# Performance work log

Measured on AMD Instinct MI355X. Metric: run time of the kernel, lower is better.

The kernel has to match this reference:

```python
import jax, jax.numpy as jnp
import numpy as np

B, S, H = 2, 1024, 2048
NH, NKV, HD = 16, 8, 128
GROUPS = NH // NKV
THETA = 1000000.0
SPARSITY = 0.4  # q_len > 512 -> vision_sparse_attention_sparsity_ratio
TOP_K = max(1, min(S, int(SPARSITY * S)))


def _rope(q, k, position_ids):
    # inv_freq: [HD/2]
    inv_freq = 1.0 / (THETA ** (jnp.arange(0, HD, 2, dtype=jnp.float32) / HD))
    freqs = position_ids.astype(jnp.float32)[:, :, None] * inv_freq  # [B,S,HD/2]
    emb = jnp.concatenate([freqs, freqs], axis=-1)                   # [B,S,HD]
    cos = jnp.cos(emb)[:, None].astype(q.dtype)  # [B,1,S,HD] (unsqueeze_dim=1)
    sin = jnp.sin(emb)[:, None].astype(q.dtype)
    rot = lambda x: jnp.concatenate([-x[..., HD // 2:], x[..., :HD // 2]], axis=-1)
    return q * cos + rot(q) * sin, k * cos + rot(k) * sin


def setup_inputs() -> dict:
    key = jax.random.key(0)
    ks = jax.random.split(key, 10)
    sc = 0.02
    inp = {
        'hidden_states': jax.random.normal(ks[0], (B, S, H), jnp.float32),
        'wq': jax.random.normal(ks[1], (NH * HD, H), jnp.float32) * sc,
        'bq': jax.random.normal(ks[2], (NH * HD,), jnp.float32) * sc,
        'wk': jax.random.normal(ks[3], (NKV * HD, H), jnp.float32) * sc,
        'bk': jax.random.normal(ks[4], (NKV * HD,), jnp.float32) * sc,
        'wv': jax.random.normal(ks[5], (NKV * HD, H), jnp.float32) * sc,
        'bv': jax.random.normal(ks[6], (NKV * HD,), jnp.float32) * sc,
        'wo': jax.random.normal(ks[7], (H, NH * HD), jnp.float32) * sc,
        'bo': jax.random.normal(ks[8], (H,), jnp.float32) * sc,
        'position_ids': jnp.tile(jnp.arange(S, dtype=jnp.int32)[None, :], (B, 1)),
    }
    return inp


def reference(hidden_states, wq, bq, wk, bk, wv, bv, wo, bo, position_ids):
    # QKV projections -> [B, heads, S, HD]
    q = (hidden_states @ wq.T + bq).reshape(B, S, NH, HD).transpose(0, 2, 1, 3)
    k = (hidden_states @ wk.T + bk).reshape(B, S, NKV, HD).transpose(0, 2, 1, 3)
    v = (hidden_states @ wv.T + bv).reshape(B, S, NKV, HD).transpose(0, 2, 1, 3)

    q, k = _rope(q, k, position_ids)

    # GQA: repeat_interleave KV heads along head axis
    k = jnp.repeat(k, GROUPS, axis=1)
    v = jnp.repeat(v, GROUPS, axis=1)

    scores = jnp.einsum('bhqd,bhkd->bhqk', q, k) / jnp.sqrt(jnp.float32(HD))

    # VectorizedSparseAttention: keep top-k weights per query, -inf elsewhere
    topk_vals = jax.lax.top_k(scores, TOP_K)[0]          # sorted descending
    thresh = topk_vals[..., -1:]                         # k-th largest per row
    sparse = jnp.where(scores >= thresh, scores, -jnp.inf)

    probs = jax.nn.softmax(sparse.astype(jnp.float32), axis=-1).astype(q.dtype)
    attn = jnp.einsum('bhqk,bhkd->bhqd', probs, v)       # [B,NH,S,HD]
    attn = attn.transpose(0, 2, 1, 3).reshape(B, S, NH * HD)
    return attn @ wo.T + bo
```

## Files before the change

kernel.cpp:

```cpp
#include <hip/hip_runtime.h>
#include <hip/hip_bf16.h>

constexpr int B_ = 2, S_ = 1024, H_ = 2048;
constexpr int NH_ = 16, NKV_ = 8, HD_ = 128, GROUPS_ = 2;
constexpr int TOPK_ = 409;
constexpr int QSTRIDE = NH_ * HD_;
constexpr int KSTRIDE = NKV_ * HD_;
constexpr int QB_ = 16;

typedef __attribute__((ext_vector_type(8))) short short8;
typedef __attribute__((ext_vector_type(4))) float f32x4;
typedef __attribute__((ext_vector_type(4))) unsigned u32x4;
typedef __attribute__((ext_vector_type(4))) unsigned short ush4;

__device__ inline unsigned fkey(float x) {
  unsigned u = __float_as_uint(x);
  return (u & 0x80000000u) ? ~u : (u | 0x80000000u);
}
__device__ inline unsigned short bf16_rne(float x) {
  unsigned u = __float_as_uint(x);
  unsigned r = u + 0x7FFFu + ((u >> 16) & 1u);
  return (unsigned short)(r >> 16);
}
__device__ inline float bf16_to_f(unsigned short h) {
  return __uint_as_float((unsigned)h << 16);
}
__device__ inline unsigned packsplit(float x) {
  unsigned u = __float_as_uint(x);
  unsigned r = (u + 0x7FFFu + ((u >> 16) & 1u)) & 0xFFFF0000u;
  float rem = x - __uint_as_float(r);
  unsigned v = __float_as_uint(rem);
  unsigned l = (v + 0x7FFFu + ((v >> 16) & 1u)) >> 16;
  return r | l;
}

#define PERM_HI 0x07060302u
#define PERM_LO 0x05040100u

__device__ inline void unpack8(const unsigned* p, short8& hi, short8& lo) {
  u32x4 w0 = *(const u32x4*)p;
  u32x4 w1 = *(const u32x4*)(p + 4);
  u32x4 h, l;
  h.x = __builtin_amdgcn_perm(w0.y, w0.x, PERM_HI);
  h.y = __builtin_amdgcn_perm(w0.w, w0.z, PERM_HI);
  h.z = __builtin_amdgcn_perm(w1.y, w1.x, PERM_HI);
  h.w = __builtin_amdgcn_perm(w1.w, w1.z, PERM_HI);
  l.x = __builtin_amdgcn_perm(w0.y, w0.x, PERM_LO);
  l.y = __builtin_amdgcn_perm(w0.w, w0.z, PERM_LO);
  l.z = __builtin_amdgcn_perm(w1.y, w1.x, PERM_LO);
  l.w = __builtin_amdgcn_perm(w1.w, w1.z, PERM_LO);
  hi = *(short8*)&h;
  lo = *(short8*)&l;
}

__device__ inline void wave_lds_fence() {
  asm volatile("s_waitcnt lgkmcnt(0)" ::: "memory");
}

template <int TI>
__device__ __forceinline__ void gemm_split_body(
    const float* __restrict__ A, const float* __restrict__ W,
    const float* __restrict__ bias, float* __restrict__ C, int ldc, int c0,
    int K, int m0) {
  __shared__ unsigned short Ah[2][TI * 32 * 32];
  __shared__ unsigned short Al[2][TI * 32 * 32];
  __shared__ unsigned short Wh[2][128 * 32];
  __shared__ unsigned short Wl[2][128 * 32];
  const int tid = threadIdx.x;
  const int lane = tid & 63, wid = tid >> 6;
  const int wrow = (wid >> 1) * (TI * 16), wcol = (wid & 1) * 64;
  const int fm = lane & 15, quad = lane >> 4;
  const int srow = tid >> 3;
  const int skq = (tid & 7) * 4;
  f32x4 acc[TI][4] = {};
  float4 avr[TI], wvr[4];

  auto loadAW = [&](int k0) {
#pragma unroll
    for (int r = 0; r < TI; ++r)
      avr[r] = *(const float4*)&A[(size_t)(m0 + srow + 32 * r) * K + k0 + skq];
#pragma unroll
    for (int r = 0; r < 4; ++r)
      wvr[r] = *(const float4*)&W[(size_t)(srow + 32 * r) * K + k0 + skq];
  };
  auto convWrite = [&](int buf) {
#pragma unroll
    for (int r = 0; r < TI; ++r) {
      const int row = srow + 32 * r;
      const int off =
          row * 32 + ((((skq >> 3) ^ ((row >> 1) & 3)) << 3) | (skq & 7));
      unsigned short h0 = bf16_rne(avr[r].x), h1 = bf16_rne(avr[r].y),
                     h2 = bf16_rne(avr[r].z), h3 = bf16_rne(avr[r].w);
      ush4 hv; hv.x = h0; hv.y = h1; hv.z = h2; hv.w = h3;
      ush4 lv;
      lv.x = bf16_rne(avr[r].x - bf16_to_f(h0));
      lv.y = bf16_rne(avr[r].y - bf16_to_f(h1));
      lv.z = bf16_rne(avr[r].z - bf16_to_f(h2));
      lv.w = bf16_rne(avr[r].w - bf16_to_f(h3));
      *(ush4*)&Ah[buf][off] = hv;
      *(ush4*)&Al[buf][off] = lv;
    }
#pragma unroll
    for (int r = 0; r < 4; ++r) {
      const int row = srow + 32 * r;
      const int off =
          row * 32 + ((((skq >> 3) ^ ((row >> 1) & 3)) << 3) | (skq & 7));
      unsigned short g0 = bf16_rne(wvr[r].x), g1 = bf16_rne(wvr[r].y),
                     g2 = bf16_rne(wvr[r].z), g3 = bf16_rne(wvr[r].w);
      ush4 hv; hv.x = g0; hv.y = g1; hv.z = g2; hv.w = g3;
      ush4 lv;
      lv.x = bf16_rne(wvr[r].x - bf16_to_f(g0));
      lv.y = bf16_rne(wvr[r].y - bf16_to_f(g1));
      lv.z = bf16_rne(wvr[r].z - bf16_to_f(g2));
      lv.w = bf16_rne(wvr[r].w - bf16_to_f(g3));
      *(ush4*)&Wh[buf][off] = hv;
      *(ush4*)&Wl[buf][off] = lv;
    }
  };

  loadAW(0);
  convWrite(0);
  __syncthreads();
  int cur = 0;
  for (int k0 = 0; k0 < K; k0 += 32) {
    const bool more = (k0 + 32) < K;
    if (more) loadAW(k0 + 32);
    short8 ah[TI], al[TI], bh[4], bl[4];
#pragma unroll
    for (int ti = 0; ti < TI; ++ti) {
      const int r = wrow + 16 * ti + fm;
      const int off = r * 32 + ((quad ^ ((r >> 1) & 3)) << 3);
      ah[ti] = *(const short8*)&Ah[cur][off];
      al[ti] = *(const short8*)&Al[cur][off];
    }
#pragma unroll
    for (int tj = 0; tj < 4; ++tj) {
      const int r = wcol + 16 * tj + fm;
      const int off = r * 32 + ((quad ^ ((r >> 1) & 3)) << 3);
      bh[tj] = *(const short8*)&Wh[cur][off];
      bl[tj] = *(const short8*)&Wl[cur][off];
    }
#pragma unroll
    for (int ti = 0; ti < TI; ++ti)
#pragma unroll
      for (int tj = 0; tj < 4; ++tj) {
        acc[ti][tj] = __builtin_amdgcn_mfma_f32_16x16x32_bf16(
            ah[ti], bh[tj], acc[ti][tj], 0, 0, 0);
        acc[ti][tj] = __builtin_amdgcn_mfma_f32_16x16x32_bf16(
            ah[ti], bl[tj], acc[ti][tj], 0, 0, 0);
        acc[ti][tj] = __builtin_amdgcn_mfma_f32_16x16x32_bf16(
            al[ti], bh[tj], acc[ti][tj], 0, 0, 0);
      }
    if (more) convWrite(cur ^ 1);
    __syncthreads();
    cur ^= 1;
  }
#pragma unroll
  for (int tj = 0; tj < 4; ++tj) {
    float bsv = bias[wcol + 16 * tj + fm];
#pragma unroll
    for (int ti = 0; ti < TI; ++ti) {
      int mrow = m0 + wrow + 16 * ti + quad * 4;
      int ncol = c0 + wcol + 16 * tj + fm;
#pragma unroll
      for (int reg = 0; reg < 4; ++reg)
        C[(size_t)(mrow + reg) * ldc + ncol] = acc[ti][tj][reg] + bsv;
    }
  }
}

__global__ __launch_bounds__(256) void gemm_qkv(
    const float* __restrict__ hidden, const float* __restrict__ wq,
    const float* __restrict__ bq, const float* __restrict__ wk,
    const float* __restrict__ bk, const float* __restrict__ wv,
    const float* __restrict__ bv, float* __restrict__ q, float* __restrict__ k,
    float* __restrict__ v) {
  const int n0 = blockIdx.x * 128, m0 = blockIdx.y * 128;
  const float* W;
  const float* bias;
  float* C;
  int ldc, c0;
  if (n0 < QSTRIDE) {
    W = wq + (size_t)n0 * H_; bias = bq + n0; C = q; ldc = QSTRIDE; c0 = n0;
  } else if (n0 < QSTRIDE + KSTRIDE) {
    int nn = n0 - QSTRIDE;
    W = wk + (size_t)nn * H_; bias = bk + nn; C = k; ldc = KSTRIDE; c0 = nn;
  } else {
    int nn = n0 - QSTRIDE - KSTRIDE;
    W = wv + (size_t)nn * H_; bias = bv + nn; C = v; ldc = KSTRIDE; c0 = nn;
  }
  gemm_split_body<4>(hidden, W, bias, C, ldc, c0, H_, m0);
}

template <int TI>
__global__ __launch_bounds__(256) void gemm_split_k(
    const float* __restrict__ A, const float* __restrict__ W,
    const float* __restrict__ bias, float* __restrict__ C, int N, int K) {
  const int n0 = blockIdx.x * 128, m0 = blockIdx.y * (TI * 32);
  gemm_split_body<TI>(A, W + (size_t)n0 * K, bias + n0, C, N, n0, K, m0);
}

__global__ __launch_bounds__(256) void rope_pack(float* __restrict__ qtmp,
                                                 float* __restrict__ ktmp,
                                                 float* __restrict__ vtmp,
                                                 const int* __restrict__ pos_ids) {
  const int s = blockIdx.x, b = blockIdx.y;
  const int t = threadIdx.x;
  __shared__ float fsh[64];
  if (t < 64) fsh[t] = (float)(1.0 / pow(1.0e6, (double)t / 64.0));
  __syncthreads();
  const int pos = pos_ids[b * S_ + s];
#pragma unroll
  for (int it = 0; it < 8; ++it) {
    const int p = t + 256 * it;
    const int slot = p >> 6;
    const int d = p & 63;
    float* base;
    if (slot < NH_)
      base = qtmp + (size_t)(b * S_ + s) * QSTRIDE + slot * HD_;
    else if (slot < NH_ + NKV_)
      base = ktmp + (size_t)(b * S_ + s) * KSTRIDE + (slot - NH_) * HD_;
    else
      base = vtmp + (size_t)(b * S_ + s) * KSTRIDE + (slot - NH_ - NKV_) * HD_;
    float x = base[d], y = base[d + 64];
    unsigned* up = (unsigned*)base;
    if (slot < NH_ + NKV_) {
      float ang = (float)pos * fsh[d];
      float c = cosf(ang), sn = sinf(ang);
      up[d] = packsplit(x * c - y * sn);
      up[d + 64] = packsplit(y * c + x * sn);
    } else {
      up[d] = packsplit(x);
      up[d + 64] = packsplit(y);
    }
  }
}

constexpr int SCW = 1028;
constexpr int KVP = 132;

__global__ __launch_bounds__(512, 1) void attn_kernel(
    unsigned* __restrict__ qpk, const unsigned* __restrict__ kpk,
    const unsigned* __restrict__ vpk) {
  const int q0 = blockIdx.x * QB_;
  const int h = blockIdx.y, b = blockIdx.z, g = h / GROUPS_;
  const int t = threadIdx.x, lane = t & 63, wid = t >> 6;
  const int fm = lane & 15, quad = lane >> 4;

  __shared__ float sc[QB_ * SCW];
  __shared__ unsigned kvt[128 * KVP];
  __shared__ unsigned qst[QB_][KVP];
  __shared__ unsigned hist[8][256];
  __shared__ float redmx[8][QB_];
  __shared__ float Zsh[QB_];
  __shared__ unsigned prefix_sh[QB_];
  __shared__ unsigned selbin_sh[8];
  __shared__ int selkk_sh[8];
  const float scale = 0.08838834764831845f;

  const int kt = t >> 5;
  const int st = (t & 31) * 4;
  const int stsw = st ^ (((kt >> 3) & 1) << 4);

  {
    int qi = t >> 5, c4 = (t & 31) * 4;
    u32x4 v = *(const u32x4*)&qpk[(size_t)(b * S_ + q0 + qi) * QSTRIDE +
                                  h * HD_ + c4];
    *(u32x4*)&qst[qi][c4] = v;
  }
  const unsigned* kg = kpk + (size_t)(b * S_) * KSTRIDE + g * HD_;
  u32x4 pf[8];
#pragma unroll
  for (int j = 0; j < 8; ++j)
    pf[j] = *(const u32x4*)&kg[(size_t)(kt + 16 * j) * KSTRIDE + st];
  __syncthreads();

  short8 qh[4], ql[4];
#pragma unroll
  for (int ks = 0; ks < 4; ++ks)
    unpack8(&qst[fm][ks * 32 + quad * 8], qh[ks], ql[ks]);

  const int kswz = ((fm >> 3) & 1) << 4;
  f32x4 mxacc = {-1e30f, -1e30f, -1e30f, -1e30f};
  for (int tile = 0; tile < 8; ++tile) {
    if (tile) __syncthreads();
#pragma unroll
    for (int j = 0; j < 8; ++j)
      *(u32x4*)&kvt[(kt + 16 * j) * KVP + stsw] = pf[j];
    __syncthreads();
    if (tile < 7) {
#pragma unroll
      for (int j = 0; j < 8; ++j)
        pf[j] = *(const u32x4*)&kg[(size_t)((tile + 1) * 128 + kt + 16 * j) *
                                       KSTRIDE + st];
    }
    f32x4 acc = {0.f, 0.f, 0.f, 0.f};
    const int krow = wid * 16 + fm;
#pragma unroll
    for (int ks = 0; ks < 4; ++ks) {
      short8 bh, bl;
      unpack8(&kvt[krow * KVP + ((ks * 32 + quad * 8) ^ kswz)], bh, bl);
      acc = __builtin_amdgcn_mfma_f32_16x16x32_bf16(qh[ks], bh, acc, 0, 0, 0);
      acc = __builtin_amdgcn_mfma_f32_16x16x32_bf16(qh[ks], bl, acc, 0, 0, 0);
      acc = __builtin_amdgcn_mfma_f32_16x16x32_bf16(ql[ks], bh, acc, 0, 0, 0);
    }
    const int key = tile * 128 + krow;
#pragma unroll
    for (int reg = 0; reg < 4; ++reg) {
      float sval = acc[reg] * scale;
      sc[(quad * 4 + reg) * SCW + key] = sval;
      mxacc[reg] = fmaxf(mxacc[reg], sval);
    }
  }
#pragma unroll
  for (int o = 1; o < 16; o <<= 1) {
    mxacc[0] = fmaxf(mxacc[0], __shfl_xor(mxacc[0], o));
    mxacc[1] = fmaxf(mxacc[1], __shfl_xor(mxacc[1], o));
    mxacc[2] = fmaxf(mxacc[2], __shfl_xor(mxacc[2], o));
    mxacc[3] = fmaxf(mxacc[3], __shfl_xor(mxacc[3], o));
  }
  if (fm == 0) {
#pragma unroll
    for (int reg = 0; reg < 4; ++reg) redmx[wid][quad * 4 + reg] = mxacc[reg];
  }
  __syncthreads();

  const unsigned* vg = vpk + (size_t)(b * S_) * KSTRIDE + g * HD_;
  u32x4 vf[8];
#pragma unroll
  for (int j = 0; j < 8; ++j)
    vf[j] = *(const u32x4*)&vg[(size_t)(kt + 16 * j) * KSTRIDE + st];

  for (int sq = 0; sq < 2; ++sq) {
    const int qi = wid * 2 + sq;
    int kk = TOPK_;
    unsigned prefix = 0;
    for (int pass = 0; pass < 4; ++pass) {
      const int shift = 24 - 8 * pass;
      const unsigned pmask = pass ? (0xFFFFFFFFu << (shift + 8)) : 0u;
      *(u32x4*)&hist[wid][4 * lane] = (u32x4){0, 0, 0, 0};
      wave_lds_fence();
#pragma unroll 4
      for (int j = 0; j < 16; ++j) {
        unsigned u = fkey(sc[qi * SCW + lane + 64 * j]);
        if ((u & pmask) == (prefix & pmask))
          atomicAdd(&hist[wid][(u >> shift) & 255], 1u);
      }
      wave_lds_fence();
      u32x4 cw = *(const u32x4*)&hist[wid][4 * lane];
      int c0 = (int)cw.x, c1 = (int)cw.y, c2 = (int)cw.z, c3 = (int)cw.w;
      int s3 = c3, s2 = c2 + s3, s1 = c1 + s2, s0 = c0 + s1;
      int tot = s0;
      int suf = tot;
#pragma unroll
      for (int off = 1; off < 64; off <<= 1) {
        int vv = __shfl_down(suf, off);
        if (lane + off < 64) suf += vv;
      }
      int above_lanes = suf - tot;
      int i0 = s0 + above_lanes, i1 = s1 + above_lanes;
      int i2 = s2 + above_lanes, i3 = s3 + above_lanes;
      if (i3 >= kk && i3 - c3 < kk) {
        selbin_sh[wid] = (unsigned)(4 * lane + 3); selkk_sh[wid] = kk - (i3 - c3);
      }
      if (i2 >= kk && i2 - c2 < kk) {
        selbin_sh[wid] = (unsigned)(4 * lane + 2); selkk_sh[wid] = kk - (i2 - c2);
      }
      if (i1 >= kk && i1 - c1 < kk) {
        selbin_sh[wid] = (unsigned)(4 * lane + 1); selkk_sh[wid] = kk - (i1 - c1);
      }
      if (i0 >= kk && i0 - c0 < kk) {
        selbin_sh[wid] = (unsigned)(4 * lane + 0); selkk_sh[wid] = kk - (i0 - c0);
      }
      wave_lds_fence();
      prefix |= selbin_sh[wid] << shift;
      kk = selkk_sh[wid];
    }
    if (lane == 0) prefix_sh[qi] = prefix;
  }
  wave_lds_fence();

  {
    const int qi = t >> 5, li = t & 31;
    const float mx =
        fmaxf(fmaxf(fmaxf(redmx[0][qi], redmx[1][qi]),
                    fmaxf(redmx[2][qi], redmx[3][qi])),
              fmaxf(fmaxf(redmx[4][qi], redmx[5][qi]),
                    fmaxf(redmx[6][qi], redmx[7][qi])));
    const unsigned pref = prefix_sh[qi];
    unsigned* scp = (unsigned*)&sc[qi * SCW];
    float zloc = 0.f;
#pragma unroll 2
    for (int j = 0; j < 8; ++j) {
      int i4 = li * 4 + 128 * j;
      f32x4 sv = *(const f32x4*)&sc[qi * SCW + i4];
      u32x4 pk;
      float p0 = (fkey(sv.x) >= pref) ? __expf(sv.x - mx) : 0.0f;
      float p1 = (fkey(sv.y) >= pref) ? __expf(sv.y - mx) : 0.0f;
      float p2 = (fkey(sv.z) >= pref) ? __expf(sv.z - mx) : 0.0f;
      float p3 = (fkey(sv.w) >= pref) ? __expf(sv.w - mx) : 0.0f;
      zloc += p0 + p1 + p2 + p3;
      pk.x = packsplit(p0); pk.y = packsplit(p1);
      pk.z = packsplit(p2); pk.w = packsplit(p3);
      *(u32x4*)&scp[i4] = pk;
    }
#pragma unroll
    for (int off = 1; off < 32; off <<= 1) zloc += __shfl_xor(zloc, off);
    if (li == 0) Zsh[qi] = zloc;
  }

  const unsigned* scp2 = (const unsigned*)sc;
  f32x4 oacc = {0.f, 0.f, 0.f, 0.f};
  const int dim = wid * 16 + fm;
  for (int tile = 0; tile < 8; ++tile) {
    __syncthreads();
#pragma unroll
    for (int j = 0; j < 8; ++j)
      *(u32x4*)&kvt[(kt + 16 * j) * KVP + stsw] = vf[j];
    __syncthreads();
    if (tile < 7) {
#pragma unroll
      for (int j = 0; j < 8; ++j)
        vf[j] = *(const u32x4*)&vg[(size_t)((tile + 1) * 128 + kt + 16 * j) *
                                       KSTRIDE + st];
    }
    const int dsw = dim ^ ((quad & 1) << 4);
#pragma unroll
    for (int ks = 0; ks < 4; ++ks) {
      short8 ph, pl;
      unpack8(&scp2[fm * SCW + tile * 128 + ks * 32 + quad * 8], ph, pl);
      const int rb = ks * 32 + quad * 8;
      unsigned w0 = kvt[(rb + 0) * KVP + dsw];
      unsigned w1 = kvt[(rb + 1) * KVP + dsw];
      unsigned w2 = kvt[(rb + 2) * KVP + dsw];
      unsigned w3 = kvt[(rb + 3) * KVP + dsw];
      unsigned w4 = kvt[(rb + 4) * KVP + dsw];
      unsigned w5 = kvt[(rb + 5) * KVP + dsw];
      unsigned w6 = kvt[(rb + 6) * KVP + dsw];
      unsigned w7 = kvt[(rb + 7) * KVP + dsw];
      u32x4 hq, lq;
      hq.x = __builtin_amdgcn_perm(w1, w0, PERM_HI);
      hq.y = __builtin_amdgcn_perm(w3, w2, PERM_HI);
      hq.z = __builtin_amdgcn_perm(w5, w4, PERM_HI);
      hq.w = __builtin_amdgcn_perm(w7, w6, PERM_HI);
      lq.x = __builtin_amdgcn_perm(w1, w0, PERM_LO);
      lq.y = __builtin_amdgcn_perm(w3, w2, PERM_LO);
      lq.z = __builtin_amdgcn_perm(w5, w4, PERM_LO);
      lq.w = __builtin_amdgcn_perm(w7, w6, PERM_LO);
      short8 vh = *(short8*)&hq;
      short8 vl = *(short8*)&lq;
      oacc = __builtin_amdgcn_mfma_f32_16x16x32_bf16(ph, vh, oacc, 0, 0, 0);
      oacc = __builtin_amdgcn_mfma_f32_16x16x32_bf16(ph, vl, oacc, 0, 0, 0);
      oacc = __builtin_amdgcn_mfma_f32_16x16x32_bf16(pl, vh, oacc, 0, 0, 0);
    }
  }

#pragma unroll
  for (int reg = 0; reg < 4; ++reg) {
    const int q = quad * 4 + reg;
    const float invZ = 1.0f / Zsh[q];
    float* outp = (float*)qpk + (size_t)(b * S_ + q0 + q) * QSTRIDE + h * HD_;
    outp[dim] = oacc[reg] * invZ;
  }
}

extern "C" void kernel_launch(void* const* d_in, const int* in_sizes, int n_in,
                              void* d_out, int out_size, void* d_ws,
                              size_t ws_size, hipStream_t stream) {
  const float* hidden = (const float*)d_in[0];
  const float* wq = (const float*)d_in[1];
  const float* bq = (const float*)d_in[2];
  const float* wk = (const float*)d_in[3];
  const float* bk = (const float*)d_in[4];
  const float* wv = (const float*)d_in[5];
  const float* bv = (const float*)d_in[6];
  const float* wo = (const float*)d_in[7];
  const float* bo = (const float*)d_in[8];
  const int* pos = (const int*)d_in[9];
  float* out = (float*)d_out;

  char* ws = (char*)d_ws;
  float* qtmp = (float*)ws;
  float* ktmp = (float*)(ws + ((size_t)16 << 20));
  float* vtmp = (float*)(ws + ((size_t)24 << 20));

  dim3 blk(256);
  gemm_qkv<<<dim3(32, 16), blk, 0, stream>>>(hidden, wq, bq, wk, bk, wv, bv,
                                             qtmp, ktmp, vtmp);
  rope_pack<<<dim3(S_, B_), dim3(256), 0, stream>>>(qtmp, ktmp, vtmp, pos);
  attn_kernel<<<dim3(S_ / QB_, NH_, B_), dim3(512), 0, stream>>>(
      (unsigned*)qtmp, (const unsigned*)ktmp, (const unsigned*)vtmp);
  gemm_split_k<2><<<dim3(H_ / 128, (B_ * S_) / 64), blk, 0, stream>>>(
      qtmp, wo, bo, out, H_, H_);
}
```

Before: 598.9 us.

## Load Q/K/V fragments directly from global memory, drop LDS staging, raise occupancy

Removes the shared-memory staging buffers for Q, K tiles and V tiles. Each lane now loads its MFMA operand fragments straight from global memory into registers, with V loaded as strided scalar words and double-buffered across k-steps. This frees LDS and drops per-tile barriers, and launch bounds are raised to allow more blocks per CU. In exchange, global loads are less coalesced and K/V rows are re-read from L2 by every wave.

New measurement: 592.7 us. About the same (-1.0%).

```diff
diff --git a/kernel.cpp b/kernel.cpp
--- a/kernel.cpp
+++ b/kernel.cpp
@@ -40,6 +40,19 @@
 __device__ inline void unpack8(const unsigned* p, short8& hi, short8& lo) {
   u32x4 w0 = *(const u32x4*)p;
   u32x4 w1 = *(const u32x4*)(p + 4);
+  u32x4 h, l;
+  h.x = __builtin_amdgcn_perm(w0.y, w0.x, PERM_HI);
+  h.y = __builtin_amdgcn_perm(w0.w, w0.z, PERM_HI);
+  h.z = __builtin_amdgcn_perm(w1.y, w1.x, PERM_HI);
+  h.w = __builtin_amdgcn_perm(w1.w, w1.z, PERM_HI);
+  l.x = __builtin_amdgcn_perm(w0.y, w0.x, PERM_LO);
+  l.y = __builtin_amdgcn_perm(w0.w, w0.z, PERM_LO);
+  l.z = __builtin_amdgcn_perm(w1.y, w1.x, PERM_LO);
+  l.w = __builtin_amdgcn_perm(w1.w, w1.z, PERM_LO);
+  hi = *(short8*)&h;
+  lo = *(short8*)&l;
+}
+__device__ inline void unpack8r(u32x4 w0, u32x4 w1, short8& hi, short8& lo) {
   u32x4 h, l;
   h.x = __builtin_amdgcn_perm(w0.y, w0.x, PERM_HI);
   h.y = __builtin_amdgcn_perm(w0.w, w0.z, PERM_HI);
@@ -236,10 +249,9 @@
   }
 }
 
-constexpr int SCW = 1028;
-constexpr int KVP = 132;
-
-__global__ __launch_bounds__(512, 1) void attn_kernel(
+constexpr int SCW = 1030;
+
+__global__ __launch_bounds__(512, 4) void attn_kernel(
     unsigned* __restrict__ qpk, const unsigned* __restrict__ kpk,
     const unsigned* __restrict__ vpk) {
   const int q0 = blockIdx.x * QB_;
@@ -248,8 +260,6 @@
   const int fm = lane & 15, quad = lane >> 4;
 
   __shared__ float sc[QB_ * SCW];
-  __shared__ unsigned kvt[128 * KVP];
-  __shared__ unsigned qst[QB_][KVP];
   __shared__ unsigned hist[8][256];
   __shared__ float redmx[8][QB_];
   __shared__ float Zsh[QB_];
@@ -258,53 +268,38 @@
   __shared__ int selkk_sh[8];
   const float scale = 0.08838834764831845f;
 
-  const int kt = t >> 5;
-  const int st = (t & 31) * 4;
-  const int stsw = st ^ (((kt >> 3) & 1) << 4);
-
+  short8 qh[4], ql[4];
   {
-    int qi = t >> 5, c4 = (t & 31) * 4;
-    u32x4 v = *(const u32x4*)&qpk[(size_t)(b * S_ + q0 + qi) * QSTRIDE +
-                                  h * HD_ + c4];
-    *(u32x4*)&qst[qi][c4] = v;
-  }
+    const unsigned* qrow =
+        qpk + (size_t)(b * S_ + q0 + fm) * QSTRIDE + h * HD_;
+#pragma unroll
+    for (int ks = 0; ks < 4; ++ks) {
+      u32x4 a0 = *(const u32x4*)&qrow[ks * 32 + quad * 8];
+      u32x4 a1 = *(const u32x4*)&qrow[ks * 32 + quad * 8 + 4];
+      unpack8r(a0, a1, qh[ks], ql[ks]);
+    }
+  }
+
   const unsigned* kg = kpk + (size_t)(b * S_) * KSTRIDE + g * HD_;
-  u32x4 pf[8];
-#pragma unroll
-  for (int j = 0; j < 8; ++j)
-    pf[j] = *(const u32x4*)&kg[(size_t)(kt + 16 * j) * KSTRIDE + st];
-  __syncthreads();
-
-  short8 qh[4], ql[4];
-#pragma unroll
-  for (int ks = 0; ks < 4; ++ks)
-    unpack8(&qst[fm][ks * 32 + quad * 8], qh[ks], ql[ks]);
-
-  const int kswz = ((fm >> 3) & 1) << 4;
   f32x4 mxacc = {-1e30f, -1e30f, -1e30f, -1e30f};
   for (int tile = 0; tile < 8; ++tile) {
-    if (tile) __syncthreads();
-#pragma unroll
-    for (int j = 0; j < 8; ++j)
-      *(u32x4*)&kvt[(kt + 16 * j) * KVP + stsw] = pf[j];
-    __syncthreads();
-    if (tile < 7) {
-#pragma unroll
-      for (int j = 0; j < 8; ++j)
-        pf[j] = *(const u32x4*)&kg[(size_t)((tile + 1) * 128 + kt + 16 * j) *
-                                       KSTRIDE + st];
+    const unsigned* kr = kg + (size_t)(tile * 128 + wid * 16 + fm) * KSTRIDE;
+    u32x4 kreg[8];
+#pragma unroll
+    for (int ks = 0; ks < 4; ++ks) {
+      kreg[2 * ks] = *(const u32x4*)&kr[ks * 32 + quad * 8];
+      kreg[2 * ks + 1] = *(const u32x4*)&kr[ks * 32 + quad * 8 + 4];
     }
     f32x4 acc = {0.f, 0.f, 0.f, 0.f};
-    const int krow = wid * 16 + fm;
 #pragma unroll
     for (int ks = 0; ks < 4; ++ks) {
       short8 bh, bl;
-      unpack8(&kvt[krow * KVP + ((ks * 32 + quad * 8) ^ kswz)], bh, bl);
+      unpack8r(kreg[2 * ks], kreg[2 * ks + 1], bh, bl);
       acc = __builtin_amdgcn_mfma_f32_16x16x32_bf16(qh[ks], bh, acc, 0, 0, 0);
       acc = __builtin_amdgcn_mfma_f32_16x16x32_bf16(qh[ks], bl, acc, 0, 0, 0);
       acc = __builtin_amdgcn_mfma_f32_16x16x32_bf16(ql[ks], bh, acc, 0, 0, 0);
     }
-    const int key = tile * 128 + krow;
+    const int key = tile * 128 + wid * 16 + fm;
 #pragma unroll
     for (int reg = 0; reg < 4; ++reg) {
       float sval = acc[reg] * scale;
@@ -324,12 +319,6 @@
     for (int reg = 0; reg < 4; ++reg) redmx[wid][quad * 4 + reg] = mxacc[reg];
   }
   __syncthreads();
-
-  const unsigned* vg = vpk + (size_t)(b * S_) * KSTRIDE + g * HD_;
-  u32x4 vf[8];
-#pragma unroll
-  for (int j = 0; j < 8; ++j)
-    vf[j] = *(const u32x4*)&vg[(size_t)(kt + 16 * j) * KSTRIDE + st];
 
   for (int sq = 0; sq < 2; ++sq) {
     const int qi = wid * 2 + sq;
@@ -408,51 +397,47 @@
     for (int off = 1; off < 32; off <<= 1) zloc += __shfl_xor(zloc, off);
     if (li == 0) Zsh[qi] = zloc;
   }
+  __syncthreads();
 
   const unsigned* scp2 = (const unsigned*)sc;
+  const unsigned* vg = vpk + (size_t)(b * S_) * KSTRIDE + g * HD_;
   f32x4 oacc = {0.f, 0.f, 0.f, 0.f};
   const int dim = wid * 16 + fm;
+
+  auto pvstep = [&](const unsigned* w, int tile, int ksv) {
+    short8 ph, pl;
+    unpack8(&scp2[fm * SCW + tile * 128 + ksv * 32 + quad * 8], ph, pl);
+    u32x4 hq, lq;
+    hq.x = __builtin_amdgcn_perm(w[1], w[0], PERM_HI);
+    hq.y = __builtin_amdgcn_perm(w[3], w[2], PERM_HI);
+    hq.z = __builtin_amdgcn_perm(w[5], w[4], PERM_HI);
+    hq.w = __builtin_amdgcn_perm(w[7], w[6], PERM_HI);
+    lq.x = __builtin_amdgcn_perm(w[1], w[0], PERM_LO);
+    lq.y = __builtin_amdgcn_perm(w[3], w[2], PERM_LO);
+    lq.z = __builtin_amdgcn_perm(w[5], w[4], PERM_LO);
+    lq.w = __builtin_amdgcn_perm(w[7], w[6], PERM_LO);
+    short8 vh = *(short8*)&hq;
+    short8 vl = *(short8*)&lq;
+    oacc = __builtin_amdgcn_mfma_f32_16x16x32_bf16(ph, vh, oacc, 0, 0, 0);
+    oacc = __builtin_amdgcn_mfma_f32_16x16x32_bf16(ph, vl, oacc, 0, 0, 0);
+    oacc = __builtin_amdgcn_mfma_f32_16x16x32_bf16(pl, vh, oacc, 0, 0, 0);
+  };
+
   for (int tile = 0; tile < 8; ++tile) {
-    __syncthreads();
-#pragma unroll
-    for (int j = 0; j < 8; ++j)
-      *(u32x4*)&kvt[(kt + 16 * j) * KVP + stsw] = vf[j];
-    __syncthreads();
-    if (tile < 7) {
-#pragma unroll
-      for (int j = 0; j < 8; ++j)
-        vf[j] = *(const u32x4*)&vg[(size_t)((tile + 1) * 128 + kt + 16 * j) *
-                                       KSTRIDE + st];
-    }
-    const int dsw = dim ^ ((quad & 1) << 4);
-#pragma unroll
-    for (int ks = 0; ks < 4; ++ks) {
-      short8 ph, pl;
-      unpack8(&scp2[fm * SCW + tile * 128 + ks * 32 + quad * 8], ph, pl);
-      const int rb = ks * 32 + quad * 8;
-      unsigned w0 = kvt[(rb + 0) * KVP + dsw];
-      unsigned w1 = kvt[(rb + 1) * KVP + dsw];
-      unsigned w2 = kvt[(rb + 2) * KVP + dsw];
-      unsigned w3 = kvt[(rb + 3) * KVP + dsw];
-      unsigned w4 = kvt[(rb + 4) * KVP + dsw];
-      unsigned w5 = kvt[(rb + 5) * KVP + dsw];
-      unsigned w6 = kvt[(rb + 6) * KVP + dsw];
-      unsigned w7 = kvt[(rb + 7) * KVP + dsw];
-      u32x4 hq, lq;
-      hq.x = __builtin_amdgcn_perm(w1, w0, PERM_HI);
-      hq.y = __builtin_amdgcn_perm(w3, w2, PERM_HI);
-      hq.z = __builtin_amdgcn_perm(w5, w4, PERM_HI);
-      hq.w = __builtin_amdgcn_perm(w7, w6, PERM_HI);
-      lq.x = __builtin_amdgcn_perm(w1, w0, PERM_LO);
-      lq.y = __builtin_amdgcn_perm(w3, w2, PERM_LO);
-      lq.z = __builtin_amdgcn_perm(w5, w4, PERM_LO);
-      lq.w = __builtin_amdgcn_perm(w7, w6, PERM_LO);
-      short8 vh = *(short8*)&hq;
-      short8 vl = *(short8*)&lq;
-      oacc = __builtin_amdgcn_mfma_f32_16x16x32_bf16(ph, vh, oacc, 0, 0, 0);
-      oacc = __builtin_amdgcn_mfma_f32_16x16x32_bf16(ph, vl, oacc, 0, 0, 0);
-      oacc = __builtin_amdgcn_mfma_f32_16x16x32_bf16(pl, vh, oacc, 0, 0, 0);
-    }
+    const unsigned* vb0 = vg + (size_t)(tile * 128 + quad * 8) * KSTRIDE + dim;
+    unsigned va[8], vb[8];
+#pragma unroll
+    for (int i = 0; i < 8; ++i) va[i] = vb0[(size_t)i * KSTRIDE];
+#pragma unroll
+    for (int i = 0; i < 8; ++i) vb[i] = vb0[(size_t)(32 + i) * KSTRIDE];
+    pvstep(va, tile, 0);
+#pragma unroll
+    for (int i = 0; i < 8; ++i) va[i] = vb0[(size_t)(64 + i) * KSTRIDE];
+    pvstep(vb, tile, 1);
+#pragma unroll
+    for (int i = 0; i < 8; ++i) vb[i] = vb0[(size_t)(96 + i) * KSTRIDE];
+    pvstep(va, tile, 2);
+    pvstep(vb, tile, 3);
   }
 
 #pragma unroll
```
